# Performance work log

Hardware: AMD Instinct MI355X
Metric: run time of the kernel (lower is better)

The kernel has to match this reference:

```python
import jax, jax.numpy as jnp
import numpy as np

GAMMA = 0.9
TEMPERATURE = 0.07
BASE_TEMPERATURE = 0.07
U_SIZE = 15_000_000
BSZ, N_VIEWS, DIM = 2048, 2, 256


def setup_inputs() -> dict:
    key = jax.random.key(0)
    kf, = jax.random.split(key, 1)
    feats = jax.random.normal(kf, (BSZ, N_VIEWS, DIM), dtype=jnp.float32)
    # contrastive features are unit-normalized in practice
    feats = feats / jnp.linalg.norm(feats, axis=-1, keepdims=True)
    index = jnp.arange(BSZ, dtype=jnp.int64) if jax.config.jax_enable_x64 else jnp.arange(BSZ, dtype=jnp.int32)
    u = jnp.zeros((U_SIZE, 1), dtype=jnp.float32)
    return {"index": index, "features": feats, "u": u}


def reference(index, features, u):
    B, V, D = features.shape          # bsz, n_views, dim
    N = B * V
    eye_b = jnp.eye(B, dtype=jnp.float32)

    # torch.cat(torch.unbind(features, dim=1), dim=0) -> [V*B, D], views stacked
    contrast_feature = jnp.transpose(features, (1, 0, 2)).reshape(N, D)
    anchor_feature = contrast_feature  # contrast_mode == 'all'

    # [N, N] similarity logits
    anchor_dot_contrast = jnp.matmul(anchor_feature, contrast_feature.T) / TEMPERATURE
    logits_max = jax.lax.stop_gradient(jnp.max(anchor_dot_contrast, axis=1, keepdims=True))
    logits = anchor_dot_contrast - logits_max

    # positive mask: tiled identity with self-contrast removed
    mask = jnp.tile(eye_b, (V, V))
    logits_mask = 1.0 - jnp.eye(N, dtype=jnp.float32)  # scatter of zeros on the diagonal
    pos_mask = mask * logits_mask
    neg_mask = 1.0 - pos_mask

    # detached negative exp-logits (EMA statistics)
    neg_exp_logits = jax.lax.stop_gradient(jnp.exp(logits) * neg_mask)

    # indexed EMA buffer update: u[index] = (1-g)*u[index] + g*rowsum[:B]
    row_sum = jnp.sum(neg_exp_logits, axis=1, keepdims=True)[:B]   # [B, 1]
    u_new = (1.0 - GAMMA) * u[index] + GAMMA * row_sum             # [B, 1]
    # (buffer write: u = u.at[index].set(u_new); only u_new is read below)

    p_neg_pairs = neg_exp_logits / jnp.tile(u_new, (V, 1))         # [N, N], detached numer/denom
    log_prob = logits - jnp.sum(p_neg_pairs * logits * neg_mask, axis=1, keepdims=True)

    mean_log_prob_pos = jnp.sum(pos_mask * log_prob, axis=1) / jnp.sum(pos_mask, axis=1)
    loss = -(TEMPERATURE / BASE_TEMPERATURE) * mean_log_prob_pos
    return loss.reshape(V, B).mean()
```

## Files before the change

### kernel.cpp

```cpp
#include <hip/hip_runtime.h>


#define BSZ   2048
#define NROW  4096
#define NB64  64
#define NT2   (NB64 * (NB64 + 1) / 2)
#define C1    (1.4426950408889634f / 0.07f)
#define LN2   0.6931471805599453f

typedef __attribute__((ext_vector_type(8))) __bf16 bf16x8;
typedef __attribute__((ext_vector_type(4))) float f32x4;

__device__ __forceinline__ const float* crow_ptr(const float* feats, int i) {
    return feats + (((i & (BSZ - 1)) * 2 + (i >> 11)) << 8);
}

__device__ __forceinline__ bf16x8 cvt8(float4 a, float4 b) {
    bf16x8 r;
    r[0] = (__bf16)a.x; r[1] = (__bf16)a.y; r[2] = (__bf16)a.z; r[3] = (__bf16)a.w;
    r[4] = (__bf16)b.x; r[5] = (__bf16)b.y; r[6] = (__bf16)b.z; r[7] = (__bf16)b.w;
    return r;
}

__global__ __launch_bounds__(64, 2) void gemm_fused(const float* __restrict__ feats,
        float* __restrict__ E, float* __restrict__ W2, float* __restrict__ Lpos) {
    int lane = threadIdx.x;
    int quad = lane >> 4;
    int l15  = lane & 15;

    int t = blockIdx.x;
    int p = (int)((sqrtf(8.0f * (float)t + 1.0f) - 1.0f) * 0.5f);
    while ((p + 1) * (p + 2) / 2 <= t) ++p;
    while (p * (p + 1) / 2 > t) --p;
    int q = t - p * (p + 1) / 2;
    int rowBase = q << 6;
    int colBase = p << 6;
    bool offdiag = (p != q);

    const float* aB = crow_ptr(feats, rowBase + l15) + (quad << 3);
    const float* bB = crow_ptr(feats, colBase + l15) + (quad << 3);

    f32x4 acc[4][4];
    #pragma unroll
    for (int a = 0; a < 4; ++a)
        #pragma unroll
        for (int c = 0; c < 4; ++c) acc[a][c] = (f32x4){0.f, 0.f, 0.f, 0.f};

    float4 rA[4][2], rB[4][2];
    #pragma unroll
    for (int rt = 0; rt < 4; ++rt) {
        rA[rt][0] = *(const float4*)(aB + rt * 8192);
        rA[rt][1] = *(const float4*)(aB + rt * 8192 + 4);
        rB[rt][0] = *(const float4*)(bB + rt * 8192);
        rB[rt][1] = *(const float4*)(bB + rt * 8192 + 4);
    }

    #pragma unroll
    for (int k = 0; k < 8; ++k) {
        bf16x8 fa[4], fb[4];
        #pragma unroll
        for (int rt = 0; rt < 4; ++rt) {
            fa[rt] = cvt8(rA[rt][0], rA[rt][1]);
            fb[rt] = cvt8(rB[rt][0], rB[rt][1]);
        }
        if (k < 7) {
            #pragma unroll
            for (int rt = 0; rt < 4; ++rt) {
                rA[rt][0] = *(const float4*)(aB + rt * 8192 + (k + 1) * 32);
                rA[rt][1] = *(const float4*)(aB + rt * 8192 + (k + 1) * 32 + 4);
                rB[rt][0] = *(const float4*)(bB + rt * 8192 + (k + 1) * 32);
                rB[rt][1] = *(const float4*)(bB + rt * 8192 + (k + 1) * 32 + 4);
            }
        }
        #pragma unroll
        for (int rt = 0; rt < 4; ++rt)
            #pragma unroll
            for (int ct = 0; ct < 4; ++ct)
                acc[rt][ct] = __builtin_amdgcn_mfma_f32_16x16x32_bf16(
                    fa[rt], fb[ct], acc[rt][ct], 0, 0, 0);
    }

    float Ep[4][4] = {}, Wp[4][4] = {};
    float Ec[4] = {}, Wc[4] = {};
    #pragma unroll
    for (int rt = 0; rt < 4; ++rt) {
        #pragma unroll
        for (int ct = 0; ct < 4; ++ct) {
            #pragma unroll
            for (int r = 0; r < 4; ++r) {
                float d = acc[rt][ct][r];
                float tt = __builtin_fmaf(d, C1, -C1);
                float e = __builtin_exp2f(tt);
                Ep[rt][r] += e;
                Wp[rt][r] = __builtin_fmaf(e, tt, Wp[rt][r]);
                if (offdiag) {
                    Ec[ct] += e;
                    Wc[ct] = __builtin_fmaf(e, tt, Wc[ct]);
                }
            }
        }
    }

    if (p == (q ^ 32)) {
        if (quad == (l15 >> 2)) {
            int r = l15 & 3;
            #pragma unroll
            for (int rt = 0; rt < 4; ++rt) {
                float lp = __builtin_fmaf(acc[rt][rt][r], C1, -C1);
                Lpos[rowBase + rt * 16 + l15] = lp;
                Lpos[colBase + rt * 16 + l15] = lp;
            }
        }
    }

    #pragma unroll
    for (int rt = 0; rt < 4; ++rt) {
        #pragma unroll
        for (int r = 0; r < 4; ++r) {
            float e = Ep[rt][r], w = Wp[rt][r];
            #pragma unroll
            for (int off = 1; off < 16; off <<= 1) {
                e += __shfl_xor(e, off, 64);
                w += __shfl_xor(w, off, 64);
            }
            if (l15 == 0) {
                int grow = rowBase + rt * 16 + (quad << 2) + r;
                atomicAdd(&E[grow], e);
                atomicAdd(&W2[grow], w);
            }
        }
    }
    if (offdiag) {
        #pragma unroll
        for (int ct = 0; ct < 4; ++ct) {
            float e = Ec[ct], w = Wc[ct];
            e += __shfl_xor(e, 16, 64);  w += __shfl_xor(w, 16, 64);
            e += __shfl_xor(e, 32, 64);  w += __shfl_xor(w, 32, 64);
            if (quad == 0) {
                int gcol = colBase + ct * 16 + l15;
                atomicAdd(&E[gcol], e);
                atomicAdd(&W2[gcol], w);
            }
        }
    }
}

__global__ __launch_bounds__(1024) void finalize_kernel(const int* __restrict__ index,
        const float* __restrict__ u, const float* __restrict__ E,
        const float* __restrict__ W2, const float* __restrict__ Lpos,
        float* __restrict__ out) {
    __shared__ float unew[BSZ];
    __shared__ float partial[16];
    int tid = threadIdx.x;
    for (int b = tid; b < BSZ; b += 1024) {
        float tp = Lpos[b];
        unew[b] = 0.1f * u[index[b]] + 0.9f * (E[b] - __builtin_exp2f(tp));
    }
    __syncthreads();
    float local = 0.0f;
    for (int i = tid; i < NROW; i += 1024) {
        float tp  = Lpos[i];
        float etp = __builtin_exp2f(tp);
        local += tp - (W2[i] - etp * tp) / unew[i & (BSZ - 1)];
    }
    #pragma unroll
    for (int off = 32; off; off >>= 1) local += __shfl_xor(local, off, 64);
    if ((tid & 63) == 0) partial[tid >> 6] = local;
    __syncthreads();
    if (tid == 0) {
        float s = 0.0f;
        #pragma unroll
        for (int w = 0; w < 16; ++w) s += partial[w];
        out[0] = -LN2 * s / (float)NROW;
    }
}

extern "C" void kernel_launch(void* const* d_in, const int* in_sizes, int n_in,
                              void* d_out, int out_size, void* d_ws, size_t ws_size,
                              hipStream_t stream) {
    const int*   index = (const int*)d_in[0];
    const float* feats = (const float*)d_in[1];
    const float* u     = (const float*)d_in[2];
    float* out = (float*)d_out;

    float* E    = (float*)d_ws;
    float* W2   = E + NROW;
    float* Lpos = W2 + NROW;

    hipMemsetAsync(E, 0, 2 * NROW * sizeof(float), stream);
    gemm_fused<<<NT2, 64, 0, stream>>>(feats, E, W2, Lpos);
    finalize_kernel<<<1, 1024, 0, stream>>>(index, u, E, W2, Lpos, out);
}
```

Before: 136.7 us.

## Stage accumulator tile in LDS for row/column reductions instead of shuffles

Writes the 64x64 MFMA accumulator tile to padded shared memory. Each lane then reduces one full row, and for off-diagonal tiles one full column, to produce the exp and weighted sums. This replaces the per-fragment cross-lane shuffle reductions and cuts the many atomics down to one per lane per output. It also drops the register double-buffered prefetch of the next K slice and uses a non-unrolled K loop. That lowers register pressure but exposes global load latency, and it adds about 17KB of LDS per block.

Measured after the change: 137.0 us. About the same (+0.2%).

```diff
diff --git a/kernel.cpp b/kernel.cpp
--- a/kernel.cpp
+++ b/kernel.cpp
@@ -7,6 +7,7 @@
 #define NT2   (NB64 * (NB64 + 1) / 2)
 #define C1    (1.4426950408889634f / 0.07f)
 #define LN2   0.6931471805599453f
+#define SROW  66
 
 typedef __attribute__((ext_vector_type(8))) __bf16 bf16x8;
 typedef __attribute__((ext_vector_type(4))) float f32x4;
@@ -24,6 +25,7 @@
 
 __global__ __launch_bounds__(64, 2) void gemm_fused(const float* __restrict__ feats,
         float* __restrict__ E, float* __restrict__ W2, float* __restrict__ Lpos) {
+    __shared__ float sacc[64 * SROW];
     int lane = threadIdx.x;
     int quad = lane >> 4;
     int l15  = lane & 15;
@@ -46,31 +48,19 @@
         #pragma unroll
         for (int c = 0; c < 4; ++c) acc[a][c] = (f32x4){0.f, 0.f, 0.f, 0.f};
 
-    float4 rA[4][2], rB[4][2];
-    #pragma unroll
-    for (int rt = 0; rt < 4; ++rt) {
-        rA[rt][0] = *(const float4*)(aB + rt * 8192);
-        rA[rt][1] = *(const float4*)(aB + rt * 8192 + 4);
-        rB[rt][0] = *(const float4*)(bB + rt * 8192);
-        rB[rt][1] = *(const float4*)(bB + rt * 8192 + 4);
-    }
-
-    #pragma unroll
+    #pragma unroll 1
     for (int k = 0; k < 8; ++k) {
+        const float* ak = aB + (k << 5);
+        const float* bk = bB + (k << 5);
         bf16x8 fa[4], fb[4];
         #pragma unroll
         for (int rt = 0; rt < 4; ++rt) {
-            fa[rt] = cvt8(rA[rt][0], rA[rt][1]);
-            fb[rt] = cvt8(rB[rt][0], rB[rt][1]);
-        }
-        if (k < 7) {
-            #pragma unroll
-            for (int rt = 0; rt < 4; ++rt) {
-                rA[rt][0] = *(const float4*)(aB + rt * 8192 + (k + 1) * 32);
-                rA[rt][1] = *(const float4*)(aB + rt * 8192 + (k + 1) * 32 + 4);
-                rB[rt][0] = *(const float4*)(bB + rt * 8192 + (k + 1) * 32);
-                rB[rt][1] = *(const float4*)(bB + rt * 8192 + (k + 1) * 32 + 4);
-            }
+            float4 x0 = *(const float4*)(ak + rt * 8192);
+            float4 x1 = *(const float4*)(ak + rt * 8192 + 4);
+            float4 y0 = *(const float4*)(bk + rt * 8192);
+            float4 y1 = *(const float4*)(bk + rt * 8192 + 4);
+            fa[rt] = cvt8(x0, x1);
+            fb[rt] = cvt8(y0, y1);
         }
         #pragma unroll
         for (int rt = 0; rt < 4; ++rt)
@@ -80,68 +70,59 @@
                     fa[rt], fb[ct], acc[rt][ct], 0, 0, 0);
     }
 
-    float Ep[4][4] = {}, Wp[4][4] = {};
-    float Ec[4] = {}, Wc[4] = {};
-    #pragma unroll
-    for (int rt = 0; rt < 4; ++rt) {
+    {
+        int wbase = (quad << 2) * SROW + l15;
         #pragma unroll
-        for (int ct = 0; ct < 4; ++ct) {
+        for (int rt = 0; rt < 4; ++rt)
             #pragma unroll
-            for (int r = 0; r < 4; ++r) {
-                float d = acc[rt][ct][r];
-                float tt = __builtin_fmaf(d, C1, -C1);
+            for (int ct = 0; ct < 4; ++ct)
+                #pragma unroll
+                for (int r = 0; r < 4; ++r)
+                    sacc[wbase + ((rt << 4) + r) * SROW + (ct << 4)] = acc[rt][ct][r];
+    }
+
+    float eS = 0.0f, wS = 0.0f;
+    float* myrow = &sacc[lane * SROW];
+    #pragma unroll 1
+    for (int j = 0; j < 16; ++j) {
+        float4 d = *(float4*)&myrow[j << 2];
+        float4 tt;
+        tt.x = __builtin_fmaf(d.x, C1, -C1);
+        tt.y = __builtin_fmaf(d.y, C1, -C1);
+        tt.z = __builtin_fmaf(d.z, C1, -C1);
+        tt.w = __builtin_fmaf(d.w, C1, -C1);
+        float e0 = __builtin_exp2f(tt.x), e1 = __builtin_exp2f(tt.y);
+        float e2 = __builtin_exp2f(tt.z), e3 = __builtin_exp2f(tt.w);
+        eS += (e0 + e1) + (e2 + e3);
+        wS = __builtin_fmaf(e0, tt.x, wS);
+        wS = __builtin_fmaf(e1, tt.y, wS);
+        wS = __builtin_fmaf(e2, tt.z, wS);
+        wS = __builtin_fmaf(e3, tt.w, wS);
+        *(float4*)&myrow[j << 2] = tt;
+    }
+    atomicAdd(&E[rowBase + lane], eS);
+    atomicAdd(&W2[rowBase + lane], wS);
+
+    if (p == (q ^ 32)) {
+        float lp = sacc[lane * (SROW + 1)];
+        Lpos[rowBase + lane] = lp;
+        Lpos[colBase + lane] = lp;
+    }
+
+    if (offdiag) {
+        float eC = 0.0f, wC = 0.0f;
+        #pragma unroll 1
+        for (int j = 0; j < 16; ++j) {
+            #pragma unroll
+            for (int jj = 0; jj < 4; ++jj) {
+                float tt = sacc[((j << 2) + jj) * SROW + lane];
                 float e = __builtin_exp2f(tt);
-                Ep[rt][r] += e;
-                Wp[rt][r] = __builtin_fmaf(e, tt, Wp[rt][r]);
-                if (offdiag) {
-                    Ec[ct] += e;
-                    Wc[ct] = __builtin_fmaf(e, tt, Wc[ct]);
-                }
+                eC += e;
+                wC = __builtin_fmaf(e, tt, wC);
             }
         }
-    }
-
-    if (p == (q ^ 32)) {
-        if (quad == (l15 >> 2)) {
-            int r = l15 & 3;
-            #pragma unroll
-            for (int rt = 0; rt < 4; ++rt) {
-                float lp = __builtin_fmaf(acc[rt][rt][r], C1, -C1);
-                Lpos[rowBase + rt * 16 + l15] = lp;
-                Lpos[colBase + rt * 16 + l15] = lp;
-            }
-        }
-    }
-
-    #pragma unroll
-    for (int rt = 0; rt < 4; ++rt) {
-        #pragma unroll
-        for (int r = 0; r < 4; ++r) {
-            float e = Ep[rt][r], w = Wp[rt][r];
-            #pragma unroll
-            for (int off = 1; off < 16; off <<= 1) {
-                e += __shfl_xor(e, off, 64);
-                w += __shfl_xor(w, off, 64);
-            }
-            if (l15 == 0) {
-                int grow = rowBase + rt * 16 + (quad << 2) + r;
-                atomicAdd(&E[grow], e);
-                atomicAdd(&W2[grow], w);
-            }
-        }
-    }
-    if (offdiag) {
-        #pragma unroll
-        for (int ct = 0; ct < 4; ++ct) {
-            float e = Ec[ct], w = Wc[ct];
-            e += __shfl_xor(e, 16, 64);  w += __shfl_xor(w, 16, 64);
-            e += __shfl_xor(e, 32, 64);  w += __shfl_xor(w, 32, 64);
-            if (quad == 0) {
-                int gcol = colBase + ct * 16 + l15;
-                atomicAdd(&E[gcol], e);
-                atomicAdd(&W2[gcol], w);
-            }
-        }
+        atomicAdd(&E[colBase + lane], eC);
+        atomicAdd(&W2[colBase + lane], wC);
     }
 }
 
```
